# Kernel optimization log

Measured on AMD Instinct MI355X. Metric: run time of the kernel, lower is better.

## Reference

```python
import jax, jax.numpy as jnp
import numpy as np

EMB = 1024
NH = 16
HS = EMB // NH

def setup_inputs() -> dict:
    key = jax.random.key(0)
    ks = jax.random.split(key, 9)
    s = 0.02
    x = jax.random.normal(ks[0], (4, 2048, EMB), dtype=jnp.float32)
    Wq = jax.random.normal(ks[1], (EMB, EMB), dtype=jnp.float32) * s
    bq = jnp.zeros((EMB,), jnp.float32)
    Wk = jax.random.normal(ks[2], (EMB, EMB), dtype=jnp.float32) * s
    bk = jnp.zeros((EMB,), jnp.float32)
    Wv = jax.random.normal(ks[3], (EMB, EMB), dtype=jnp.float32) * s
    bv = jnp.zeros((EMB,), jnp.float32)
    Wo = jax.random.normal(ks[4], (EMB, EMB), dtype=jnp.float32) * s
    bo = jnp.zeros((EMB,), jnp.float32)
    return {"x": x, "Wq": Wq, "bq": bq, "Wk": Wk, "bk": bk,
            "Wv": Wv, "bv": bv, "Wo": Wo, "bo": bo}

def reference(x, Wq, bq, Wk, bk, Wv, bv, Wo, bo):
    B, T, C = x.shape
    q = x @ Wq + bq
    k = x @ Wk + bk
    v = x @ Wv + bv
    # [B, H, T, hs]
    q = q.reshape(B, T, NH, HS).transpose(0, 2, 1, 3)
    k = k.reshape(B, T, NH, HS).transpose(0, 2, 1, 3)
    v = v.reshape(B, T, NH, HS).transpose(0, 2, 1, 3)
    scale = 1.0 / np.sqrt(HS).astype(np.float32)
    att = jnp.einsum('bhqd,bhkd->bhqk', q, k) * scale
    causal = jnp.tril(jnp.ones((T, T), dtype=bool))
    att = jnp.where(causal[None, None], att, jnp.float32(-jnp.inf))
    att = jax.nn.softmax(att, axis=-1)
    y = jnp.einsum('bhqk,bhkd->bhqd', att, v)
    y = y.transpose(0, 2, 1, 3).reshape(B, T, C)
    return y @ Wo + bo
```

## Files before the change

### kernel.cpp

```cpp
#include <hip/hip_runtime.h>

#define EMB   1024
#define NHEAD 16
#define HS    64
#define BATCH 4
#define SEQ   2048
#define MTOK  (BATCH*SEQ)

typedef __bf16 bf16;
typedef __bf16 bf16x8 __attribute__((ext_vector_type(8)));
typedef __bf16 bf16x4 __attribute__((ext_vector_type(4)));
typedef float  f32x4  __attribute__((ext_vector_type(4)));
typedef _Float16 f16;
typedef f16 f16x4 __attribute__((ext_vector_type(4)));
typedef f16 f16x8 __attribute__((ext_vector_type(8)));

#define MFMA16(a,b,c)     __builtin_amdgcn_mfma_f32_16x16x32_bf16(a,b,c,0,0,0)
#define MFMA_H32(a,b,c)   __builtin_amdgcn_mfma_f32_16x16x32_f16(a,b,c,0,0,0)
#define MFMA_H16(a,b,c)   __builtin_amdgcn_mfma_f32_16x16x16f16(a,b,c,0,0,0)

#if __has_builtin(__builtin_amdgcn_exp2f)
#define EXP2(x) __builtin_amdgcn_exp2f(x)
#else
#define EXP2(x) exp2f(x)
#endif

#define GLL(g, l) __builtin_amdgcn_global_load_lds(                         \
        (const __attribute__((address_space(1))) void*)(g),                 \
        (__attribute__((address_space(3))) void*)(l), 16, 0, 0)

__global__ __launch_bounds__(256) void k_prep(
        const float* __restrict__ x, bf16* __restrict__ xb,
        const float* __restrict__ W0, const float* __restrict__ W1,
        const float* __restrict__ W2, const float* __restrict__ W3,
        bf16* __restrict__ T0, bf16* __restrict__ T1,
        bf16* __restrict__ T2, bf16* __restrict__ T3) {
    const int z = blockIdx.z;
    if (z == 0) {
        const int blk = blockIdx.y * 16 + blockIdx.x;
        const size_t base = (size_t)blk * 32768;
        for (int j = threadIdx.x; j < 8192; j += 256) {
            size_t i = base + (size_t)j * 4;
            float4 v = *(const float4*)(x + i);
            bf16x4 o;
            o[0] = (bf16)v.x; o[1] = (bf16)v.y; o[2] = (bf16)v.z; o[3] = (bf16)v.w;
            *(bf16x4*)(xb + i) = o;
        }
        return;
    }
    __shared__ float tile[64][65];
    const float* W = (z == 1) ? W0 : (z == 2) ? W1 : (z == 3) ? W2 : W3;
    bf16* Wt = (z == 1) ? T0 : (z == 2) ? T1 : (z == 3) ? T2 : T3;
    int c0 = blockIdx.x * 64, r0 = blockIdx.y * 64;
    int tx = threadIdx.x & 63, ty = threadIdx.x >> 6;
    #pragma unroll
    for (int r = ty; r < 64; r += 4)
        tile[r][tx] = W[(r0 + r) * EMB + c0 + tx];
    __syncthreads();
    #pragma unroll
    for (int cc = ty; cc < 64; cc += 4)
        Wt[(c0 + cc) * EMB + r0 + tx] = (bf16)tile[tx][cc];
}

__global__ __launch_bounds__(512, 2) void k_qkv_gemm(
        const bf16* __restrict__ xb,
        const bf16* __restrict__ Wall,
        const float* __restrict__ bq, const float* __restrict__ bk, const float* __restrict__ bv,
        f16* __restrict__ Q, f16* __restrict__ K, f16* __restrict__ Vt) {
    __shared__ __align__(16) bf16 As[2][8192];
    __shared__ __align__(16) bf16 Bs[2][6144];
    const int tid = threadIdx.x;
    const int lane = tid & 63;
    const int l15 = lane & 15, quad = lane >> 4;
    const int wave = tid >> 6;
    const int wm4 = wave & 3;
    const int wn2 = wave >> 2;

    const int mt = blockIdx.x;
    const int nt = blockIdx.y;
    const int n0 = nt * 192;

    const bf16* Abase = xb   + (size_t)mt * 256 * EMB;
    const bf16* Bbase = Wall + (size_t)n0 * EMB;

    const int P   = tid >> 3, s8 = tid & 7;
    const int cch = s8 ^ (P & 7);
    const int r_  = 2 * P + (cch >> 2);
    const int kc8 = (cch & 3) * 8;
    const bf16* Asrc = Abase + (size_t)r_ * EMB + kc8;
    const bf16* Bsrc = Bbase + (size_t)r_ * EMB + kc8;

#define STAGE_A(T, cb) do {                                                  \
    GLL(Asrc + (T) * 32,             &As[cb][tid * 8]);                      \
    GLL(Asrc + 128 * EMB + (T) * 32, &As[cb][tid * 8 + 4096]); } while (0)
#define STAGE_B(T, cb) do {                                                  \
    GLL(Bsrc + (T) * 32,             &Bs[cb][tid * 8]);                      \
    if (tid < 256)                                                           \
        GLL(Bsrc + 128 * EMB + (T) * 32, &Bs[cb][tid * 8 + 4096]);           \
} while (0)

    int aoff[4], boff[6];
    #pragma unroll
    for (int mf = 0; mf < 4; mf++) {
        const int row = wm4 * 64 + mf * 16 + l15;
        const int Pr = row >> 1, hh = row & 1;
        aoff[mf] = Pr * 64 + ((((hh << 2) | quad)) ^ (Pr & 7)) * 8;
    }
    #pragma unroll
    for (int nf = 0; nf < 6; nf++) {
        const int row = wn2 * 96 + nf * 16 + l15;
        const int Pr = row >> 1, hh = row & 1;
        boff[nf] = Pr * 64 + ((((hh << 2) | quad)) ^ (Pr & 7)) * 8;
    }

    f32x4 acc[4][6];
    #pragma unroll
    for (int i = 0; i < 4; i++)
        #pragma unroll
        for (int j = 0; j < 6; j++) acc[i][j] = (f32x4){0.f, 0.f, 0.f, 0.f};

#define BARX __builtin_amdgcn_s_barrier()
#define PRI1 __builtin_amdgcn_s_setprio(1)
#define PRI0 __builtin_amdgcn_s_setprio(0)
#define SCHB __builtin_amdgcn_sched_barrier(0)
#define VM0 asm volatile("s_waitcnt vmcnt(0)" ::: "memory")

    STAGE_A(0, 0); STAGE_B(0, 0);
    SCHB; VM0; BARX;

    bf16x8 a[4], b[3], b2[3];
    #pragma unroll 1
    for (int W = 0; W < 31; ++W) {
        const int c = W & 1;
        const bf16* Ab = As[c];
        const bf16* Bb = Bs[c];
        #pragma unroll
        for (int i = 0; i < 4; i++) a[i] = *(const bf16x8*)(Ab + aoff[i]);
        #pragma unroll
        for (int j = 0; j < 3; j++) b[j] = *(const bf16x8*)(Bb + boff[j]);
        STAGE_A(W + 1, c ^ 1);
        SCHB;
        BARX; PRI1;
        #pragma unroll
        for (int i = 0; i < 4; i++)
            #pragma unroll
            for (int j = 0; j < 3; j++)
                acc[i][j] = MFMA16(a[i], b[j], acc[i][j]);
        PRI0;
        #pragma unroll
        for (int j = 0; j < 3; j++) b2[j] = *(const bf16x8*)(Bb + boff[3 + j]);
        STAGE_B(W + 1, c ^ 1);
        SCHB; VM0; BARX;
        PRI1;
        #pragma unroll
        for (int i = 0; i < 4; i++)
            #pragma unroll
            for (int j = 0; j < 3; j++)
                acc[i][3 + j] = MFMA16(a[i], b2[j], acc[i][3 + j]);
        PRI0;
    }
    {
        const bf16* Ab = As[1];
        const bf16* Bb = Bs[1];
        #pragma unroll
        for (int i = 0; i < 4; i++) a[i] = *(const bf16x8*)(Ab + aoff[i]);
        #pragma unroll
        for (int j = 0; j < 3; j++) b[j]  = *(const bf16x8*)(Bb + boff[j]);
        #pragma unroll
        for (int j = 0; j < 3; j++) b2[j] = *(const bf16x8*)(Bb + boff[3 + j]);
        #pragma unroll
        for (int i = 0; i < 4; i++)
            #pragma unroll
            for (int j = 0; j < 3; j++) {
                acc[i][j]     = MFMA16(a[i], b[j],  acc[i][j]);
                acc[i][3 + j] = MFMA16(a[i], b2[j], acc[i][3 + j]);
            }
    }
#undef STAGE_A
#undef STAGE_B

    const float QSCALE = 0.18033688011112043f;
    #pragma unroll
    for (int nf = 0; nf < 6; nf++) {
        const int col = n0 + wn2 * 96 + nf * 16 + l15;
        const int whichf = col >> 10;
        const int cc = col & 1023;
        const int h = cc >> 6, d = cc & 63;
        const float bv_ = (whichf == 0) ? bq[cc] : (whichf == 1) ? bk[cc] : bv[cc];
        if (whichf == 2) {
            #pragma unroll
            for (int mf = 0; mf < 4; mf++) {
                const int row0 = mt * 256 + wm4 * 64 + mf * 16 + quad * 4;
                const int b_ = row0 >> 11, tk0 = row0 & (SEQ - 1);
                f16x4 vv;
                #pragma unroll
                for (int r = 0; r < 4; r++) vv[r] = (f16)(acc[mf][nf][r] + bv_);
                *(f16x4*)(Vt + (((size_t)(b_ * NHEAD + h) * 32 + (tk0 >> 6)) * 64 + d) * 64
                          + (tk0 & 63)) = vv;
            }
        } else {
            f16* OUT = (whichf == 0) ? Q : K;
            const float scl = (whichf == 0) ? QSCALE : 1.0f;
            #pragma unroll
            for (int mf = 0; mf < 4; mf++) {
                const int row0 = mt * 256 + wm4 * 64 + mf * 16 + quad * 4;
                const int b_ = row0 >> 11, tk0 = row0 & (SEQ - 1);
                #pragma unroll
                for (int r = 0; r < 4; r++)
                    OUT[((size_t)(b_ * NHEAD + h) * SEQ + (tk0 + r)) * HS + d] =
                        (f16)((acc[mf][nf][r] + bv_) * scl);
            }
        }
    }
}

__global__ __launch_bounds__(256) void k_attn(
        const f16* __restrict__ Q, const f16* __restrict__ K,
        const f16* __restrict__ Vt, bf16* __restrict__ y) {
    __shared__ __align__(16) f16 kbuf[2][64 * 64];
    __shared__ __align__(16) f16 vbuf[2][64 * 64];
    const int tid = threadIdx.x;
    const int wave = tid >> 6, lane = tid & 63;
    const int l15 = lane & 15, quad = lane >> 4;

    const int L = blockIdx.x;
    const int xcd = L & 7, s = L >> 3;
    const int bh = xcd * 8 + (s & 7);
    const int qt = 15 - (s >> 3);
    const int h = bh & (NHEAD - 1), b_ = bh >> 4;

    const f16* Qb = Q + (size_t)bh * SEQ * HS;
    const f16* Kb = K + (size_t)bh * SEQ * HS;
    const f16* Vb = Vt + (size_t)bh * 32 * 4096;

    const int c0 = tid, c1 = tid + 256;
    const int soff0 = (c0 >> 3) * 64 + (((c0 & 7) ^ ((c0 >> 3) & 7)) * 8);
    const int soff1 = (c1 >> 3) * 64 + (((c1 & 7) ^ ((c1 >> 3) & 7)) * 8);
    const int swz = l15 & 7;

    f16x4 ones;
    #pragma unroll
    for (int i = 0; i < 4; i++) ones[i] = (f16)1.0f;

    const int ntiles = 2 * qt + 2;
    const int qrow0 = qt * 128 + wave * 32;

    f16x8 qb[2][2];
    #pragma unroll
    for (int qf = 0; qf < 2; qf++)
        #pragma unroll
        for (int dk = 0; dk < 2; dk++)
            qb[qf][dk] = *(const f16x8*)(Qb + (qrow0 + 16 * qf + l15) * HS + 32 * dk + quad * 8);

    f32x4 o[2][4], lacc[2];
    #pragma unroll
    for (int qf = 0; qf < 2; qf++) {
        lacc[qf] = (f32x4){0.f, 0.f, 0.f, 0.f};
        #pragma unroll
        for (int df = 0; df < 4; df++) o[qf][df] = (f32x4){0.f, 0.f, 0.f, 0.f};
    }

    f16x8 kr0 = *(const f16x8*)(Kb + c0 * 8);
    f16x8 kr1 = *(const f16x8*)(Kb + c1 * 8);
    f16x8 vr0 = *(const f16x8*)(Vb + c0 * 8);
    f16x8 vr1 = *(const f16x8*)(Vb + c1 * 8);
    *(f16x8*)(kbuf[0] + soff0) = kr0;
    *(f16x8*)(kbuf[0] + soff1) = kr1;
    *(f16x8*)(vbuf[0] + soff0) = vr0;
    *(f16x8*)(vbuf[0] + soff1) = vr1;

    for (int it = 0; it < ntiles; ++it) {
        const int kv0 = it * 64;
        __syncthreads();
        if (it + 1 < ntiles) {
            const f16* kg = Kb + (size_t)(kv0 + 64) * HS;
            const f16* vg = Vb + (size_t)(it + 1) * 4096;
            kr0 = *(const f16x8*)(kg + c0 * 8);
            kr1 = *(const f16x8*)(kg + c1 * 8);
            vr0 = *(const f16x8*)(vg + c0 * 8);
            vr1 = *(const f16x8*)(vg + c1 * 8);
        }
        if (kv0 <= qrow0 + 31) {
            const f16* kb_ = kbuf[it & 1];
            const f16* vb_ = vbuf[it & 1];

            f32x4 sreg[4][2];
            #pragma unroll
            for (int mb = 0; mb < 4; mb++) {
                f16x8 ka0 = *(const f16x8*)(kb_ + (16 * mb + l15) * 64 + ((quad ^ swz) * 8));
                f16x8 ka1 = *(const f16x8*)(kb_ + (16 * mb + l15) * 64 + (((4 + quad) ^ swz) * 8));
                #pragma unroll
                for (int qf = 0; qf < 2; qf++) {
                    f32x4 t = (f32x4){0.f, 0.f, 0.f, 0.f};
                    t = MFMA_H32(ka0, qb[qf][0], t);
                    t = MFMA_H32(ka1, qb[qf][1], t);
                    sreg[mb][qf] = t;
                }
            }

            f16x4 pa[4][2];
            const bool edge = (kv0 + 63 > qrow0);
            #pragma unroll
            for (int mb = 0; mb < 4; mb++)
                #pragma unroll
                for (int qf = 0; qf < 2; qf++) {
                    f16x4 p;
                    if (edge) {
                        #pragma unroll
                        for (int r = 0; r < 4; r++) {
                            const int kvc = kv0 + 16 * mb + quad * 4 + r;
                            const int qq  = qrow0 + 16 * qf + l15;
                            p[r] = (f16)((kvc <= qq) ? EXP2(sreg[mb][qf][r]) : 0.f);
                        }
                    } else {
                        #pragma unroll
                        for (int r = 0; r < 4; r++)
                            p[r] = (f16)EXP2(sreg[mb][qf][r]);
                    }
                    pa[mb][qf] = p;
                }

            #pragma unroll
            for (int df = 0; df < 4; df++)
                #pragma unroll
                for (int kb = 0; kb < 4; kb++) {
                    f16x4 vfrag = *(const f16x4*)(vb_ + (16 * df + l15) * 64 +
                                    (((2 * kb + (quad >> 1)) ^ swz) * 8) + (quad & 1) * 4);
                    #pragma unroll
                    for (int qf = 0; qf < 2; qf++)
                        o[qf][df] = MFMA_H16(pa[kb][qf], vfrag, o[qf][df]);
                }
            #pragma unroll
            for (int kb = 0; kb < 4; kb++)
                #pragma unroll
                for (int qf = 0; qf < 2; qf++)
                    lacc[qf] = MFMA_H16(pa[kb][qf], ones, lacc[qf]);
        }
        if (it + 1 < ntiles) {
            const int nb = (it + 1) & 1;
            *(f16x8*)(kbuf[nb] + soff0) = kr0;
            *(f16x8*)(kbuf[nb] + soff1) = kr1;
            *(f16x8*)(vbuf[nb] + soff0) = vr0;
            *(f16x8*)(vbuf[nb] + soff1) = vr1;
        }
    }

    #pragma unroll
    for (int qf = 0; qf < 2; qf++)
        #pragma unroll
        for (int r = 0; r < 4; r++) {
            float inv = 1.f / lacc[qf][r];
            int t = qrow0 + 16 * qf + quad * 4 + r;
            bf16* yp = y + ((size_t)(b_ * SEQ + t)) * EMB + h * HS;
            #pragma unroll
            for (int df = 0; df < 4; df++)
                yp[df * 16 + l15] = (bf16)(o[qf][df][r] * inv);
        }
}

__global__ __launch_bounds__(256) void k_out_gemm(
        const bf16* __restrict__ y, const bf16* __restrict__ Wot,
        const float* __restrict__ bo, float* __restrict__ out) {
    __shared__ __align__(16) bf16 As[128 * 64];
    __shared__ __align__(16) bf16 Bs[128 * 64];
    const int tid = threadIdx.x;
    const int lane = tid & 63;
    const int wave = tid >> 6;
    const int l15 = lane & 15, quad = lane >> 4;
    const int wm = (wave >> 1) * 64, wn = (wave & 1) * 64;
    const int m0 = blockIdx.x * 128;
    const int n0 = blockIdx.y * 128;

    f32x4 acc[4][4];
    #pragma unroll
    for (int i = 0; i < 4; i++)
        #pragma unroll
        for (int j = 0; j < 4; j++) acc[i][j] = (f32x4){0.f, 0.f, 0.f, 0.f};

    const int r0_ = tid >> 3;
    const int kcs = ((tid & 7) ^ (r0_ & 7)) * 8;
    const bf16* Ag = y   + (size_t)m0 * EMB + r0_ * EMB + kcs;
    const bf16* Bg = Wot + (size_t)n0 * EMB + r0_ * EMB + kcs;
    const int rsw = l15 & 7;

    for (int k0 = 0; k0 < EMB; k0 += 64) {
        __syncthreads();
        #pragma unroll
        for (int g = 0; g < 4; g++) {
            GLL(Ag + 32 * g * EMB + k0, As + (tid + g * 256) * 8);
            GLL(Bg + 32 * g * EMB + k0, Bs + (tid + g * 256) * 8);
        }
        __syncthreads();

        bf16x8 af[2][4], bfr[2][4];
        #pragma unroll
        for (int h = 0; h < 2; h++) {
            #pragma unroll
            for (int rf = 0; rf < 4; rf++)
                af[h][rf] = *(const bf16x8*)(As + (wm + rf * 16 + l15) * 64 +
                                             (((4 * h + quad) ^ rsw) * 8));
            #pragma unroll
            for (int cf = 0; cf < 4; cf++)
                bfr[h][cf] = *(const bf16x8*)(Bs + (wn + cf * 16 + l15) * 64 +
                                              (((4 * h + quad) ^ rsw) * 8));
        }
        #pragma unroll
        for (int h = 0; h < 2; h++)
            #pragma unroll
            for (int rf = 0; rf < 4; rf++)
                #pragma unroll
                for (int cf = 0; cf < 4; cf++)
                    acc[rf][cf] = MFMA16(af[h][rf], bfr[h][cf], acc[rf][cf]);
    }

    #pragma unroll
    for (int cf = 0; cf < 4; cf++) {
        const int col = n0 + wn + cf * 16 + l15;
        const float bv_ = bo[col];
        #pragma unroll
        for (int rf = 0; rf < 4; rf++) {
            #pragma unroll
            for (int r = 0; r < 4; r++) {
                const int row = m0 + wm + rf * 16 + quad * 4 + r;
                out[(size_t)row * EMB + col] = acc[rf][cf][r] + bv_;
            }
        }
    }
}

extern "C" void kernel_launch(void* const* d_in, const int* in_sizes, int n_in,
                              void* d_out, int out_size, void* d_ws, size_t ws_size,
                              hipStream_t stream) {
    const float* x  = (const float*)d_in[0];
    const float* Wq = (const float*)d_in[1];
    const float* bq = (const float*)d_in[2];
    const float* Wk = (const float*)d_in[3];
    const float* bk = (const float*)d_in[4];
    const float* Wv = (const float*)d_in[5];
    const float* bv = (const float*)d_in[6];
    const float* Wo = (const float*)d_in[7];
    const float* bo = (const float*)d_in[8];
    float* out = (float*)d_out;

    char* ws = (char*)d_ws;
    bf16* xb  = (bf16*)(ws);
    bf16* Wqt = (bf16*)(ws + (16u << 20));
    bf16* Wkt = (bf16*)(ws + (18u << 20));
    bf16* Wvt = (bf16*)(ws + (20u << 20));
    bf16* Wot = (bf16*)(ws + (22u << 20));
    f16*  Q   = (f16*)(ws + (24u << 20));
    f16*  K   = (f16*)(ws + (40u << 20));
    f16*  Vt  = (f16*)(ws + (56u << 20));
    bf16* y   = (bf16*)(ws + (72u << 20));

    dim3 gp(16, 16, 5);
    k_prep<<<gp, 256, 0, stream>>>(x, xb, Wq, Wk, Wv, Wo, Wqt, Wkt, Wvt, Wot);

    dim3 g1(32, 16);
    k_qkv_gemm<<<g1, 512, 0, stream>>>(xb, Wqt, bq, bk, bv, Q, K, Vt);

    dim3 g2(1024);
    k_attn<<<g2, 256, 0, stream>>>(Q, K, Vt, y);

    dim3 g3(MTOK / 128, EMB / 128);
    k_out_gemm<<<g3, 256, 0, stream>>>(y, Wot, bo, out);
}
```

Before: 264.9 us.

## Drop LDS staging in attention; load K/V directly from global with permuted V layout

The attention kernel no longer stages K and V tiles through double-buffered shared memory with block-wide barriers. Each wave now reads its K and V fragments straight from global memory (through cache) and runs only as many KV tiles as its own causal range needs, so waves in a block no longer wait on each other. To keep the V loads contiguous, the QKV GEMM epilogue writes V-transposed with a permuted column order, so one pair of 16-byte loads yields the four MFMA fragments. This trades LDS reuse across the four waves for more redundant global and L2 traffic.

```diff
diff --git a/kernel.cpp b/kernel.cpp
--- a/kernel.cpp
+++ b/kernel.cpp
@@ -192,11 +192,13 @@
             for (int mf = 0; mf < 4; mf++) {
                 const int row0 = mt * 256 + wm4 * 64 + mf * 16 + quad * 4;
                 const int b_ = row0 >> 11, tk0 = row0 & (SEQ - 1);
+                const int t63 = tk0 & 63;
+                const int colp = ((t63 >> 2) & 3) * 16 + ((t63 >> 4) << 2);
                 f16x4 vv;
                 #pragma unroll
                 for (int r = 0; r < 4; r++) vv[r] = (f16)(acc[mf][nf][r] + bv_);
                 *(f16x4*)(Vt + (((size_t)(b_ * NHEAD + h) * 32 + (tk0 >> 6)) * 64 + d) * 64
-                          + (tk0 & 63)) = vv;
+                          + colp) = vv;
             }
         } else {
             f16* OUT = (whichf == 0) ? Q : K;
@@ -217,8 +219,6 @@
 __global__ __launch_bounds__(256) void k_attn(
         const f16* __restrict__ Q, const f16* __restrict__ K,
         const f16* __restrict__ Vt, bf16* __restrict__ y) {
-    __shared__ __align__(16) f16 kbuf[2][64 * 64];
-    __shared__ __align__(16) f16 vbuf[2][64 * 64];
     const int tid = threadIdx.x;
     const int wave = tid >> 6, lane = tid & 63;
     const int l15 = lane & 15, quad = lane >> 4;
@@ -233,17 +233,12 @@
     const f16* Kb = K + (size_t)bh * SEQ * HS;
     const f16* Vb = Vt + (size_t)bh * 32 * 4096;
 
-    const int c0 = tid, c1 = tid + 256;
-    const int soff0 = (c0 >> 3) * 64 + (((c0 & 7) ^ ((c0 >> 3) & 7)) * 8);
-    const int soff1 = (c1 >> 3) * 64 + (((c1 & 7) ^ ((c1 >> 3) & 7)) * 8);
-    const int swz = l15 & 7;
-
     f16x4 ones;
     #pragma unroll
     for (int i = 0; i < 4; i++) ones[i] = (f16)1.0f;
 
-    const int ntiles = 2 * qt + 2;
     const int qrow0 = qt * 128 + wave * 32;
+    const int myntiles = ((qrow0 + 31) >> 6) + 1;
 
     f16x8 qb[2][2];
     #pragma unroll
@@ -260,89 +255,69 @@
         for (int df = 0; df < 4; df++) o[qf][df] = (f32x4){0.f, 0.f, 0.f, 0.f};
     }
 
-    f16x8 kr0 = *(const f16x8*)(Kb + c0 * 8);
-    f16x8 kr1 = *(const f16x8*)(Kb + c1 * 8);
-    f16x8 vr0 = *(const f16x8*)(Vb + c0 * 8);
-    f16x8 vr1 = *(const f16x8*)(Vb + c1 * 8);
-    *(f16x8*)(kbuf[0] + soff0) = kr0;
-    *(f16x8*)(kbuf[0] + soff1) = kr1;
-    *(f16x8*)(vbuf[0] + soff0) = vr0;
-    *(f16x8*)(vbuf[0] + soff1) = vr1;
-
-    for (int it = 0; it < ntiles; ++it) {
+    #pragma unroll 1
+    for (int it = 0; it < myntiles; ++it) {
         const int kv0 = it * 64;
-        __syncthreads();
-        if (it + 1 < ntiles) {
-            const f16* kg = Kb + (size_t)(kv0 + 64) * HS;
-            const f16* vg = Vb + (size_t)(it + 1) * 4096;
-            kr0 = *(const f16x8*)(kg + c0 * 8);
-            kr1 = *(const f16x8*)(kg + c1 * 8);
-            vr0 = *(const f16x8*)(vg + c0 * 8);
-            vr1 = *(const f16x8*)(vg + c1 * 8);
-        }
-        if (kv0 <= qrow0 + 31) {
-            const f16* kb_ = kbuf[it & 1];
-            const f16* vb_ = vbuf[it & 1];
-
-            f32x4 sreg[4][2];
-            #pragma unroll
-            for (int mb = 0; mb < 4; mb++) {
-                f16x8 ka0 = *(const f16x8*)(kb_ + (16 * mb + l15) * 64 + ((quad ^ swz) * 8));
-                f16x8 ka1 = *(const f16x8*)(kb_ + (16 * mb + l15) * 64 + (((4 + quad) ^ swz) * 8));
-                #pragma unroll
-                for (int qf = 0; qf < 2; qf++) {
-                    f32x4 t = (f32x4){0.f, 0.f, 0.f, 0.f};
-                    t = MFMA_H32(ka0, qb[qf][0], t);
-                    t = MFMA_H32(ka1, qb[qf][1], t);
-                    sreg[mb][qf] = t;
+        const f16* kt = Kb + (size_t)kv0 * HS;
+        const f16* vt = Vb + (size_t)it * 4096;
+
+        f32x4 sreg[4][2];
+        #pragma unroll
+        for (int mb = 0; mb < 4; mb++) {
+            f16x8 ka0 = *(const f16x8*)(kt + (16 * mb + l15) * 64 + quad * 8);
+            f16x8 ka1 = *(const f16x8*)(kt + (16 * mb + l15) * 64 + 32 + quad * 8);
+            #pragma unroll
+            for (int qf = 0; qf < 2; qf++) {
+                f32x4 t = (f32x4){0.f, 0.f, 0.f, 0.f};
+                t = MFMA_H32(ka0, qb[qf][0], t);
+                t = MFMA_H32(ka1, qb[qf][1], t);
+                sreg[mb][qf] = t;
+            }
+        }
+
+        f16x4 pa[4][2];
+        const bool edge = (kv0 + 63 > qrow0);
+        #pragma unroll
+        for (int mb = 0; mb < 4; mb++)
+            #pragma unroll
+            for (int qf = 0; qf < 2; qf++) {
+                f16x4 p;
+                if (edge) {
+                    #pragma unroll
+                    for (int r = 0; r < 4; r++) {
+                        const int kvc = kv0 + 16 * mb + quad * 4 + r;
+                        const int qq  = qrow0 + 16 * qf + l15;
+                        p[r] = (f16)((kvc <= qq) ? EXP2(sreg[mb][qf][r]) : 0.f);
+                    }
+                } else {
+                    #pragma unroll
+                    for (int r = 0; r < 4; r++)
+                        p[r] = (f16)EXP2(sreg[mb][qf][r]);
                 }
-            }
-
-            f16x4 pa[4][2];
-            const bool edge = (kv0 + 63 > qrow0);
-            #pragma unroll
-            for (int mb = 0; mb < 4; mb++)
-                #pragma unroll
-                for (int qf = 0; qf < 2; qf++) {
-                    f16x4 p;
-                    if (edge) {
-                        #pragma unroll
-                        for (int r = 0; r < 4; r++) {
-                            const int kvc = kv0 + 16 * mb + quad * 4 + r;
-                            const int qq  = qrow0 + 16 * qf + l15;
-                            p[r] = (f16)((kvc <= qq) ? EXP2(sreg[mb][qf][r]) : 0.f);
-                        }
-                    } else {
-                        #pragma unroll
-                        for (int r = 0; r < 4; r++)
-                            p[r] = (f16)EXP2(sreg[mb][qf][r]);
-                    }
-                    pa[mb][qf] = p;
-                }
-
-            #pragma unroll
-            for (int df = 0; df < 4; df++)
-                #pragma unroll
-                for (int kb = 0; kb < 4; kb++) {
-                    f16x4 vfrag = *(const f16x4*)(vb_ + (16 * df + l15) * 64 +
-                                    (((2 * kb + (quad >> 1)) ^ swz) * 8) + (quad & 1) * 4);
-                    #pragma unroll
-                    for (int qf = 0; qf < 2; qf++)
-                        o[qf][df] = MFMA_H16(pa[kb][qf], vfrag, o[qf][df]);
-                }
+                pa[mb][qf] = p;
+            }
+
+        #pragma unroll
+        for (int df = 0; df < 4; df++) {
+            const f16* vrow = vt + (16 * df + l15) * 64 + quad * 16;
+            f16x8 v8a = *(const f16x8*)(vrow);
+            f16x8 v8b = *(const f16x8*)(vrow + 8);
+            f16x4 vf[4];
+            vf[0] = __builtin_shufflevector(v8a, v8a, 0, 1, 2, 3);
+            vf[1] = __builtin_shufflevector(v8a, v8a, 4, 5, 6, 7);
+            vf[2] = __builtin_shufflevector(v8b, v8b, 0, 1, 2, 3);
+            vf[3] = __builtin_shufflevector(v8b, v8b, 4, 5, 6, 7);
             #pragma unroll
             for (int kb = 0; kb < 4; kb++)
                 #pragma unroll
                 for (int qf = 0; qf < 2; qf++)
-                    lacc[qf] = MFMA_H16(pa[kb][qf], ones, lacc[qf]);
-        }
-        if (it + 1 < ntiles) {
-            const int nb = (it + 1) & 1;
-            *(f16x8*)(kbuf[nb] + soff0) = kr0;
-            *(f16x8*)(kbuf[nb] + soff1) = kr1;
-            *(f16x8*)(vbuf[nb] + soff0) = vr0;
-            *(f16x8*)(vbuf[nb] + soff1) = vr1;
-        }
+                    o[qf][df] = MFMA_H16(pa[kb][qf], vf[kb], o[qf][df]);
+        }
+        #pragma unroll
+        for (int kb = 0; kb < 4; kb++)
+            #pragma unroll
+            for (int qf = 0; qf < 2; qf++)
+                lacc[qf] = MFMA_H16(pa[kb][qf], ones, lacc[qf]);
     }
 
     #pragma unroll
```

Result: slower. 337.1 us (+27.3%).

## Double-buffer output projection GEMM with interleaved staged loads and priority hints

Applied to the files above, without the earlier changes.

Rewrites the output-projection GEMM main loop to use double-buffered LDS tiles of K=32 instead of a single buffer of K=64. It issues global-to-LDS loads for the next tile, split into A and B halves, between MFMA groups, and raises wave priority around MFMAs. The goal is to overlap memory traffic with matrix math and to cut the barrier stalls of the old load-then-compute loop. In exchange it adds more barriers per K step, a new swizzle layout and more complex indexing.

```diff
diff --git a/kernel.cpp b/kernel.cpp
--- a/kernel.cpp
+++ b/kernel.cpp
@@ -361,8 +361,8 @@
 __global__ __launch_bounds__(256) void k_out_gemm(
         const bf16* __restrict__ y, const bf16* __restrict__ Wot,
         const float* __restrict__ bo, float* __restrict__ out) {
-    __shared__ __align__(16) bf16 As[128 * 64];
-    __shared__ __align__(16) bf16 Bs[128 * 64];
+    __shared__ __align__(16) bf16 As[2][4096];
+    __shared__ __align__(16) bf16 Bs[2][4096];
     const int tid = threadIdx.x;
     const int lane = tid & 63;
     const int wave = tid >> 6;
@@ -371,47 +371,93 @@
     const int m0 = blockIdx.x * 128;
     const int n0 = blockIdx.y * 128;
 
+    const int P   = tid >> 3, s8 = tid & 7;
+    const int cch = s8 ^ (P & 7);
+    const int r_  = 2 * P + (cch >> 2);
+    const int kc8 = (cch & 3) * 8;
+    const bf16* Asrc = y   + (size_t)(m0 + r_) * EMB + kc8;
+    const bf16* Bsrc = Wot + (size_t)(n0 + r_) * EMB + kc8;
+
+#define STAGE_A(T, cb) do {                                                  \
+    GLL(Asrc + (T) * 32,            &As[cb][tid * 8]);                       \
+    GLL(Asrc + 64 * EMB + (T) * 32, &As[cb][tid * 8 + 2048]); } while (0)
+#define STAGE_B(T, cb) do {                                                  \
+    GLL(Bsrc + (T) * 32,            &Bs[cb][tid * 8]);                       \
+    GLL(Bsrc + 64 * EMB + (T) * 32, &Bs[cb][tid * 8 + 2048]); } while (0)
+
+    int aoff[4], boff[4];
+    #pragma unroll
+    for (int mf = 0; mf < 4; mf++) {
+        const int row = wm + mf * 16 + l15;
+        const int Pr = row >> 1, hh = row & 1;
+        aoff[mf] = Pr * 64 + ((((hh << 2) | quad)) ^ (Pr & 7)) * 8;
+    }
+    #pragma unroll
+    for (int nf = 0; nf < 4; nf++) {
+        const int row = wn + nf * 16 + l15;
+        const int Pr = row >> 1, hh = row & 1;
+        boff[nf] = Pr * 64 + ((((hh << 2) | quad)) ^ (Pr & 7)) * 8;
+    }
+
     f32x4 acc[4][4];
     #pragma unroll
     for (int i = 0; i < 4; i++)
         #pragma unroll
         for (int j = 0; j < 4; j++) acc[i][j] = (f32x4){0.f, 0.f, 0.f, 0.f};
 
-    const int r0_ = tid >> 3;
-    const int kcs = ((tid & 7) ^ (r0_ & 7)) * 8;
-    const bf16* Ag = y   + (size_t)m0 * EMB + r0_ * EMB + kcs;
-    const bf16* Bg = Wot + (size_t)n0 * EMB + r0_ * EMB + kcs;
-    const int rsw = l15 & 7;
-
-    for (int k0 = 0; k0 < EMB; k0 += 64) {
-        __syncthreads();
-        #pragma unroll
-        for (int g = 0; g < 4; g++) {
-            GLL(Ag + 32 * g * EMB + k0, As + (tid + g * 256) * 8);
-            GLL(Bg + 32 * g * EMB + k0, Bs + (tid + g * 256) * 8);
-        }
-        __syncthreads();
-
-        bf16x8 af[2][4], bfr[2][4];
-        #pragma unroll
-        for (int h = 0; h < 2; h++) {
-            #pragma unroll
-            for (int rf = 0; rf < 4; rf++)
-                af[h][rf] = *(const bf16x8*)(As + (wm + rf * 16 + l15) * 64 +
-                                             (((4 * h + quad) ^ rsw) * 8));
-            #pragma unroll
-            for (int cf = 0; cf < 4; cf++)
-                bfr[h][cf] = *(const bf16x8*)(Bs + (wn + cf * 16 + l15) * 64 +
-                                              (((4 * h + quad) ^ rsw) * 8));
-        }
-        #pragma unroll
-        for (int h = 0; h < 2; h++)
-            #pragma unroll
-            for (int rf = 0; rf < 4; rf++)
-                #pragma unroll
-                for (int cf = 0; cf < 4; cf++)
-                    acc[rf][cf] = MFMA16(af[h][rf], bfr[h][cf], acc[rf][cf]);
-    }
+    STAGE_A(0, 0); STAGE_B(0, 0);
+    SCHB; VM0; BARX;
+
+    bf16x8 a[4], b[2], b2[2];
+    #pragma unroll 1
+    for (int W = 0; W < 31; ++W) {
+        const int c = W & 1;
+        const bf16* Ab = As[c];
+        const bf16* Bb = Bs[c];
+        #pragma unroll
+        for (int i = 0; i < 4; i++) a[i] = *(const bf16x8*)(Ab + aoff[i]);
+        #pragma unroll
+        for (int j = 0; j < 2; j++) b[j] = *(const bf16x8*)(Bb + boff[j]);
+        STAGE_A(W + 1, c ^ 1);
+        SCHB;
+        BARX; PRI1;
+        #pragma unroll
+        for (int i = 0; i < 4; i++)
+            #pragma unroll
+            for (int j = 0; j < 2; j++)
+                acc[i][j] = MFMA16(a[i], b[j], acc[i][j]);
+        PRI0;
+        #pragma unroll
+        for (int j = 0; j < 2; j++) b2[j] = *(const bf16x8*)(Bb + boff[2 + j]);
+        STAGE_B(W + 1, c ^ 1);
+        SCHB; VM0; BARX;
+        PRI1;
+        #pragma unroll
+        for (int i = 0; i < 4; i++)
+            #pragma unroll
+            for (int j = 0; j < 2; j++)
+                acc[i][2 + j] = MFMA16(a[i], b2[j], acc[i][2 + j]);
+        PRI0;
+    }
+    {
+        const bf16* Ab = As[1];
+        const bf16* Bb = Bs[1];
+        #pragma unroll
+        for (int i = 0; i < 4; i++) a[i] = *(const bf16x8*)(Ab + aoff[i]);
+        #pragma unroll
+        for (int j = 0; j < 2; j++) b[j]  = *(const bf16x8*)(Bb + boff[j]);
+        #pragma unroll
+        for (int j = 0; j < 2; j++) b2[j] = *(const bf16x8*)(Bb + boff[2 + j]);
+        #pragma unroll
+        for (int i = 0; i < 4; i++)
+            #pragma unroll
+            for (int j = 0; j < 2; j++) {
+                acc[i][j]     = MFMA16(a[i], b[j],  acc[i][j]);
+                acc[i][2 + j] = MFMA16(a[i], b2[j], acc[i][2 + j]);
+            }
+    }
+#undef STAGE_A
+#undef STAGE_B
 
     #pragma unroll
     for (int cf = 0; cf < 4; cf++) {
```

Result: no change. 269.5 us (+1.7%).
